# Kernel optimization log

Hardware: AMD Instinct MI355X
Metric: run time of the kernel (lower is better)

## Reference

```python
import jax, jax.numpy as jnp
import numpy as np

E = 1024   # embed_dim
H = 16     # num_heads
D = E // H # head_dim
B = 2
S = 2048
YAT_EPS = 0.1


def setup_inputs() -> dict:
    key = jax.random.key(0)
    ks = jax.random.split(key, 5)
    w_scale = (6.0 / (E + E)) ** 0.5  # xavier_uniform bound
    def xavier(k):
        return jax.random.uniform(k, (E, E), jnp.float32, -w_scale, w_scale)
    return {
        "x": jax.random.normal(ks[0], (B, S, E), jnp.float32),
        "Wq": xavier(ks[1]), "bq": jnp.zeros((E,), jnp.float32),
        "Wk": xavier(ks[2]), "bk": jnp.zeros((E,), jnp.float32),
        "Wv": xavier(ks[3]), "bv": jnp.zeros((E,), jnp.float32),
        "Wo": xavier(ks[4]), "bo": jnp.zeros((E,), jnp.float32),
    }


def reference(x, Wq, bq, Wk, bk, Wv, bv, Wo, bo):
    b, s, _ = x.shape
    # Projections (Linear: x @ W + b, flax kernel layout [in, out])
    Q = x @ Wq + bq
    K = x @ Wk + bk
    V = x @ Wv + bv
    # [B, H, S, D]
    Q = Q.reshape(b, s, H, D).transpose(0, 2, 1, 3)
    K = K.reshape(b, s, H, D).transpose(0, 2, 1, 3)
    V = V.reshape(b, s, H, D).transpose(0, 2, 1, 3)
    # L2 normalize along head_dim
    Qn = Q / (jnp.linalg.norm(Q, axis=-1, keepdims=True) + 1e-8)
    Kn = K / (jnp.linalg.norm(K, axis=-1, keepdims=True) + 1e-8)
    # Yat kernel scores: (1 + <q,k>)^2 / (eps + (1 - <q,k>))
    dot = jnp.einsum("bhqd,bhkd->bhqk", Qn, Kn)
    scores = (1.0 + dot) ** 2 / (YAT_EPS + (1.0 - dot))
    # Sum-normalize (no softmax)
    attn = scores / (jnp.sum(scores, axis=-1, keepdims=True) + 1e-6)
    out = jnp.einsum("bhqk,bhkd->bhqd", attn, V)
    out = out.transpose(0, 2, 1, 3).reshape(b, s, E)
    return out @ Wo + bo
```

## Files before the change

kernel.cpp:

```cpp
#include <hip/hip_runtime.h>
#include <math.h>

#define EDIM 1024
#define NH   16
#define HD   64
#define BATCH 2
#define SEQ  2048
#define NROW (BATCH*SEQ)
#define YAT_EPS 0.1f

typedef _Float16 f16;
typedef _Float16 f16x8 __attribute__((ext_vector_type(8)));
typedef _Float16 f16x4 __attribute__((ext_vector_type(4)));
typedef float    f32x4 __attribute__((ext_vector_type(4)));

#define GLL16(gp, lp) __builtin_amdgcn_global_load_lds( \
    (const __attribute__((address_space(1))) void*)(gp), \
    (__attribute__((address_space(3))) void*)(lp), 16, 0, 0)

__global__ __launch_bounds__(256)
void cast_f16_kernel(const float* __restrict__ src, f16* __restrict__ dst)
{
    const int i = (blockIdx.x * 256 + threadIdx.x) * 4;
    const float4 v = *(const float4*)(src + i);
    f16x4 o = {(f16)v.x, (f16)v.y, (f16)v.z, (f16)v.w};
    *(f16x4*)(dst + i) = o;
}

__global__ __launch_bounds__(256)
void transcast4_kernel(const float* __restrict__ W0, const float* __restrict__ W1,
                       const float* __restrict__ W2, const float* __restrict__ W3,
                       f16* __restrict__ T0, f16* __restrict__ T1,
                       f16* __restrict__ T2, f16* __restrict__ T3)
{
    const int z = blockIdx.z;
    const float* W = (z == 0) ? W0 : (z == 1) ? W1 : (z == 2) ? W2 : W3;
    f16*         Wt = (z == 0) ? T0 : (z == 1) ? T1 : (z == 2) ? T2 : T3;

    __shared__ float T[32][33];
    const int t = threadIdx.x;
    const int r = t >> 3, c4 = (t & 7) * 4;
    const int bi = blockIdx.x * 32, bj = blockIdx.y * 32;
    const float4 v = *(const float4*)(W + (size_t)(bi + r) * 1024 + bj + c4);
    T[r][c4 + 0] = v.x; T[r][c4 + 1] = v.y; T[r][c4 + 2] = v.z; T[r][c4 + 3] = v.w;
    __syncthreads();
    f16x4 o = {(f16)T[c4 + 0][r], (f16)T[c4 + 1][r], (f16)T[c4 + 2][r], (f16)T[c4 + 3][r]};
    *(f16x4*)(Wt + (size_t)(bj + r) * 1024 + bi + c4) = o;
}

__global__ __launch_bounds__(256)
void gemm_f16(const f16* __restrict__ A,
              const f16* __restrict__ B0, const f16* __restrict__ B1, const f16* __restrict__ B2,
              const float* __restrict__ bi0, const float* __restrict__ bi1, const float* __restrict__ bi2,
              void* __restrict__ o0, void* __restrict__ o1, void* __restrict__ o2,
              int e0, int e1, int e2)
{
    __shared__ __align__(16) char lds[24576];

    const int z = blockIdx.z;
    const f16*   Bt   = (z == 0) ? B0  : (z == 1) ? B1  : B2;
    const float* bias = (z == 0) ? bi0 : (z == 1) ? bi1 : bi2;
    void*        Cout = (z == 0) ? o0  : (z == 1) ? o1  : o2;
    const int    epi  = (z == 0) ? e0  : (z == 1) ? e1  : e2;

    const int tid  = threadIdx.x;
    const int lane = tid & 63;
    const int w    = tid >> 6;
    const int cl   = lane & 15;
    const int quad = lane >> 4;
    const int wm = w & 1, wn = w >> 1;
    const int bm = blockIdx.x * 64, bn = blockIdx.y * 128;

    f16* As = (f16*)lds;
    f16* Bs = (f16*)(lds + 8192);

    const int srow = lane >> 2;
    const int scs  = (lane & 3) ^ (srow & 3);
    const f16* gA = A  + (size_t)(bm + w * 16 + srow) * 1024 + scs * 8;
    const f16* gB = Bt + (size_t)(bn + w * 32 + srow) * 1024 + scs * 8;
    f16* lA = As + w * 512;
    f16* lB = Bs + w * 1024;

    f32x4 acc[2][4];
#pragma unroll
    for (int i = 0; i < 2; ++i)
#pragma unroll
        for (int j = 0; j < 4; ++j) acc[i][j] = (f32x4){0.f, 0.f, 0.f, 0.f};

    GLL16(gA, lA);
    GLL16(gB, lB);
    GLL16(gB + 16 * 1024, lB + 512);

    const int fsw = (quad ^ (cl & 3)) * 8;

    for (int it = 0; it < 32; ++it) {
        const int buf = it & 1;
        __syncthreads();
        if (it < 31) {
            const int k0 = (it + 1) * 32;
            const int nb = buf ^ 1;
            GLL16(gA + k0, lA + nb * 2048);
            GLL16(gB + k0, lB + nb * 4096);
            GLL16(gB + 16 * 1024 + k0, lB + nb * 4096 + 512);
        }
        f16x8 af[2], bf[4];
#pragma unroll
        for (int mt = 0; mt < 2; ++mt)
            af[mt] = *(const f16x8*)(&As[buf * 2048 + (wm * 32 + mt * 16 + cl) * 32 + fsw]);
#pragma unroll
        for (int nt = 0; nt < 4; ++nt)
            bf[nt] = *(const f16x8*)(&Bs[buf * 4096 + (wn * 64 + nt * 16 + cl) * 32 + fsw]);
#pragma unroll
        for (int mt = 0; mt < 2; ++mt)
#pragma unroll
            for (int nt = 0; nt < 4; ++nt)
                acc[mt][nt] = __builtin_amdgcn_mfma_f32_16x16x32_f16(af[mt], bf[nt], acc[mt][nt], 0, 0, 0);
    }

    float bcol[4];
#pragma unroll
    for (int nt = 0; nt < 4; ++nt) bcol[nt] = bias[bn + wn * 64 + nt * 16 + cl];
#pragma unroll
    for (int mt = 0; mt < 2; ++mt)
#pragma unroll
        for (int nt = 0; nt < 4; ++nt)
#pragma unroll
            for (int rg = 0; rg < 4; ++rg) acc[mt][nt][rg] += bcol[nt];

    const int b_idx = bm >> 11, sl0 = bm & (SEQ - 1), h0 = bn >> 6;

    if (epi == 0) {
        float* C = (float*)Cout;
#pragma unroll
        for (int mt = 0; mt < 2; ++mt)
#pragma unroll
            for (int rg = 0; rg < 4; ++rg) {
                const int row = bm + wm * 32 + mt * 16 + quad * 4 + rg;
#pragma unroll
                for (int nt = 0; nt < 4; ++nt)
                    C[(size_t)row * EDIM + bn + wn * 64 + nt * 16 + cl] = acc[mt][nt][rg];
            }
    } else if (epi == 1) {
        f16* C = (f16*)Cout;
        __syncthreads();
        f16* S = (f16*)lds;
#pragma unroll
        for (int mt = 0; mt < 2; ++mt)
#pragma unroll
            for (int rg = 0; rg < 4; ++rg) {
                float ss = 0.f;
#pragma unroll
                for (int nt = 0; nt < 4; ++nt) ss += acc[mt][nt][rg] * acc[mt][nt][rg];
                ss += __shfl_xor(ss, 1); ss += __shfl_xor(ss, 2);
                ss += __shfl_xor(ss, 4); ss += __shfl_xor(ss, 8);
                const float inv = 1.0f / (sqrtf(ss) + 1e-8f);
                const int row = wm * 32 + mt * 16 + quad * 4 + rg;
#pragma unroll
                for (int nt = 0; nt < 4; ++nt) {
                    const int col = wn * 64 + nt * 16 + cl;
                    S[row * 128 + (((col >> 3) ^ (row & 15)) * 8) + (col & 7)] =
                        (f16)(acc[mt][nt][rg] * inv);
                }
            }
        __syncthreads();
#pragma unroll
        for (int i = 0; i < 4; ++i) {
            const int c = tid + i * 256;
            const int s = c >> 4, gi = c & 15;
            f16x8 v = *(const f16x8*)(&S[s * 128 + ((gi ^ (s & 15)) * 8)]);
            const int head = h0 + (gi >> 3), d8 = (gi & 7) * 8;
            *(f16x8*)(C + ((size_t)(b_idx * NH + head) * SEQ + sl0 + s) * HD + d8) = v;
        }
    } else {
        f16* C = (f16*)Cout;
        __syncthreads();
        f16* S = (f16*)lds;
#pragma unroll
        for (int mt = 0; mt < 2; ++mt) {
            const int s0 = wm * 32 + mt * 16 + quad * 4;
#pragma unroll
            for (int nt = 0; nt < 4; ++nt) {
                const int col = wn * 64 + nt * 16 + cl;
                f16x4 o = {(f16)acc[mt][nt][0], (f16)acc[mt][nt][1],
                           (f16)acc[mt][nt][2], (f16)acc[mt][nt][3]};
                *(f16x4*)(&S[col * 64 + (((s0 >> 3) ^ (col & 7)) * 8) + (s0 & 7)]) = o;
            }
        }
        __syncthreads();
#pragma unroll
        for (int i = 0; i < 4; ++i) {
            const int c = tid + i * 256;
            const int col = c >> 3, gi = c & 7;
            f16x8 v = *(const f16x8*)(&S[col * 64 + ((gi ^ (col & 7)) * 8)]);
            const int head = h0 + (col >> 6), d = col & 63;
            *(f16x8*)(C + ((size_t)(b_idx * NH + head) * HD + d) * SEQ + sl0 + gi * 8) = v;
        }
    }
}

__global__ __launch_bounds__(256)
void yat_attn(const f16* __restrict__ Qh, const f16* __restrict__ Kh,
              const f16* __restrict__ Vt, f16* __restrict__ AO)
{
    __shared__ __align__(16) char lds[53248];
    f16* KsB = (f16*)(lds + 20480);
    f16* VsB = (f16*)(lds + 36864);

    const int tid  = threadIdx.x;
    const int lane = tid & 63;
    const int w    = tid >> 6;
    const int cl   = lane & 15;
    const int quad = lane >> 4;
    const int wm = w & 1;
    const int wk = w >> 1;
    const int q0 = blockIdx.x * 128;
    const int bh = blockIdx.y;

    const f16* Qg = Qh + (size_t)bh * SEQ * HD;
    const f16* Kg = Kh + (size_t)bh * SEQ * HD;
    const f16* Vg = Vt + (size_t)bh * HD * SEQ;

    const int g8   = lane >> 3;
    const int scs  = (lane & 7) ^ g8;
    const int qrow = w * 8 + g8;
    const int krow = w * 16 + g8;

    {
        const f16* gQ = Qg + (size_t)(q0 + qrow) * HD + scs * 8;
        f16* lQ = (f16*)lds + w * 512;
#pragma unroll
        for (int it = 0; it < 4; ++it)
            GLL16(gQ + it * 32 * HD, lQ + it * 2048);
    }
    __syncthreads();
    f16x8 qf[4][2];
#pragma unroll
    for (int qt = 0; qt < 4; ++qt)
#pragma unroll
        for (int kb = 0; kb < 2; ++kb)
            qf[qt][kb] = *(const f16x8*)((f16*)lds + (wm * 64 + qt * 16 + cl) * 64 +
                                         ((kb * 4 + quad) ^ (cl & 7)) * 8);
    __syncthreads();

    f16* Pw = (f16*)(lds + w * 5120);

    f32x4 O[4][4];
    float rs[4] = {0.f, 0.f, 0.f, 0.f};
#pragma unroll
    for (int i = 0; i < 4; ++i)
#pragma unroll
        for (int j = 0; j < 4; ++j) O[i][j] = (f32x4){0.f, 0.f, 0.f, 0.f};

    const f16* gK = Kg + (size_t)krow * HD + scs * 8;
    const f16* gV = Vg + (size_t)krow * SEQ + scs * 8;
    f16* lK = KsB + w * 1024;
    f16* lV = VsB + w * 1024;

#pragma unroll
    for (int it = 0; it < 2; ++it) {
        GLL16(gK + (size_t)(it * 8) * HD, lK + it * 512);
        GLL16(gV + (size_t)(it * 8) * SEQ, lV + it * 512);
    }

    for (int t0 = 0; t0 < SEQ; t0 += 64) {
        const int buf = (t0 >> 6) & 1;
        __syncthreads();

        if (t0 + 64 < SEQ) {
            const int nb = buf ^ 1;
#pragma unroll
            for (int it = 0; it < 2; ++it) {
                GLL16(gK + (size_t)(t0 + 64 + it * 8) * HD, lK + nb * 4096 + it * 512);
                GLL16(gV + (size_t)(it * 8) * SEQ + t0 + 64, lV + nb * 4096 + it * 512);
            }
        }

        const f16* Ks = KsB + buf * 4096;
        const f16* Vs = VsB + buf * 4096;

        f32x4 s[2][4];
#pragma unroll
        for (int kt = 0; kt < 2; ++kt)
#pragma unroll
            for (int qt = 0; qt < 4; ++qt) s[kt][qt] = (f32x4){0.f, 0.f, 0.f, 0.f};
#pragma unroll
        for (int kb = 0; kb < 2; ++kb) {
            const int sw = ((kb * 4 + quad) ^ (cl & 7)) * 8;
            f16x8 af0 = *(const f16x8*)(&Ks[(wk * 32 +  0 + cl) * 64 + sw]);
            f16x8 af1 = *(const f16x8*)(&Ks[(wk * 32 + 16 + cl) * 64 + sw]);
#pragma unroll
            for (int qt = 0; qt < 4; ++qt) {
                s[0][qt] = __builtin_amdgcn_mfma_f32_16x16x32_f16(af0, qf[qt][kb], s[0][qt], 0, 0, 0);
                s[1][qt] = __builtin_amdgcn_mfma_f32_16x16x32_f16(af1, qf[qt][kb], s[1][qt], 0, 0, 0);
            }
        }

#pragma unroll
        for (int kt = 0; kt < 2; ++kt)
#pragma unroll
            for (int qt = 0; qt < 4; ++qt) {
                f16x4 pk;
                float psum = 0.f;
#pragma unroll
                for (int rg = 0; rg < 4; ++rg) {
                    const float u = (1.0f + YAT_EPS) - s[kt][qt][rg];
                    const float p = fmaf(4.41f, __builtin_amdgcn_rcpf(u), u - 4.2f);
                    psum += p;
                    pk[rg] = (f16)p;
                }
                rs[qt] += psum;
                *(f16x4*)(&Pw[(qt * 16 + cl) * 40 + kt * 16 + quad * 4]) = pk;
            }

        f16x8 pa[4];
#pragma unroll
        for (int qt = 0; qt < 4; ++qt)
            pa[qt] = *(const f16x8*)(&Pw[(qt * 16 + cl) * 40 + quad * 8]);
#pragma unroll
        for (int dn = 0; dn < 4; ++dn) {
            f16x8 vb = *(const f16x8*)(&Vs[(dn * 16 + cl) * 64 +
                                           ((wk * 4 + quad) ^ (cl & 7)) * 8]);
#pragma unroll
            for (int qt = 0; qt < 4; ++qt)
                O[qt][dn] = __builtin_amdgcn_mfma_f32_16x16x32_f16(pa[qt], vb, O[qt][dn], 0, 0, 0);
        }
    }

    __syncthreads();
    float* rs_s = (float*)lds;
    float* Ox   = (float*)(lds + 20480);

#pragma unroll
    for (int qt = 0; qt < 4; ++qt) {
        float t = rs[qt];
        t += __shfl_xor(t, 16);
        t += __shfl_xor(t, 32);
        if (quad == 0) rs_s[wk * 128 + wm * 64 + qt * 16 + cl] = t;
    }
    if (wk == 1) {
#pragma unroll
        for (int qt = 0; qt < 4; ++qt)
#pragma unroll
            for (int dn = 0; dn < 4; ++dn)
#pragma unroll
                for (int rg = 0; rg < 4; ++rg)
                    Ox[(wm * 64 + qt * 16 + quad * 4 + rg) * 64 + dn * 16 + cl] = O[qt][dn][rg];
    }
    __syncthreads();
    if (wk == 0) {
        const int b = bh >> 4, h = bh & 15;
#pragma unroll
        for (int qt = 0; qt < 4; ++qt)
#pragma unroll
            for (int rg = 0; rg < 4; ++rg) {
                const int ql = wm * 64 + qt * 16 + quad * 4 + rg;
                const float tot = rs_s[ql] + rs_s[128 + ql];
                const float inv = 1.0f / (tot + 1e-6f);
                const size_t rowoff = ((size_t)b * SEQ + q0 + ql) * EDIM + h * 64;
#pragma unroll
                for (int dn = 0; dn < 4; ++dn)
                    AO[rowoff + dn * 16 + cl] =
                        (f16)((O[qt][dn][rg] + Ox[ql * 64 + dn * 16 + cl]) * inv);
            }
    }
}

extern "C" void kernel_launch(void* const* d_in, const int* in_sizes, int n_in,
                              void* d_out, int out_size, void* d_ws, size_t ws_size,
                              hipStream_t stream)
{
    const float* x  = (const float*)d_in[0];
    const float* Wq = (const float*)d_in[1];
    const float* bq = (const float*)d_in[2];
    const float* Wk = (const float*)d_in[3];
    const float* bk = (const float*)d_in[4];
    const float* Wv = (const float*)d_in[5];
    const float* bv = (const float*)d_in[6];
    const float* Wo = (const float*)d_in[7];
    const float* bo = (const float*)d_in[8];

    char* p = (char*)d_ws;
    f16* xb  = (f16*)p;                 p += (size_t)NROW * EDIM * 2;
    f16* Wqt = (f16*)p;                 p += (size_t)EDIM * EDIM * 2;
    f16* Wkt = (f16*)p;                 p += (size_t)EDIM * EDIM * 2;
    f16* Wvt = (f16*)p;                 p += (size_t)EDIM * EDIM * 2;
    f16* Wot = (f16*)p;                 p += (size_t)EDIM * EDIM * 2;
    f16* Qhb = (f16*)p;                 p += (size_t)NROW * EDIM * 2;
    f16* Khb = (f16*)p;                 p += (size_t)NROW * EDIM * 2;
    f16* Vtb = (f16*)p;                 p += (size_t)NROW * EDIM * 2;
    f16* AOb = (f16*)p;                 p += (size_t)NROW * EDIM * 2;

    cast_f16_kernel<<<NROW * EDIM / 1024, 256, 0, stream>>>(x, xb);
    transcast4_kernel<<<dim3(32, 32, 4), 256, 0, stream>>>(Wq, Wk, Wv, Wo,
                                                           Wqt, Wkt, Wvt, Wot);

    gemm_f16<<<dim3(NROW / 64, EDIM / 128, 3), 256, 0, stream>>>(
        xb, Wqt, Wkt, Wvt, bq, bk, bv, Qhb, Khb, Vtb, 1, 1, 2);

    yat_attn<<<dim3(SEQ / 128, BATCH * NH), 256, 0, stream>>>(Qhb, Khb, Vtb, AOb);

    gemm_f16<<<dim3(NROW / 64, EDIM / 128, 1), 256, 0, stream>>>(
        AOb, Wot, Wot, Wot, bo, bo, bo, d_out, d_out, d_out, 0, 0, 0);
}
```

Measured before the change: 211.7 us.

## Template GEMM on M-tile and stage loads through registers with deeper prefetch

The GEMM kernel is templated on its M tile size. The QKV projection now uses 128-row tiles, which doubles the MFMA work per B-tile load and halves the grid, while the output projection keeps 64-row tiles. The global_load_lds direct-to-LDS path is replaced by register-staged loads that prefetch two K-steps ahead and write LDS one step ahead, with the barrier moved to the end of each iteration. This adds register pressure, and the larger tile means fewer blocks to fill the GPU.

Result: no change. 209.2 us (-1.2%).

```diff
diff --git a/kernel.cpp b/kernel.cpp
--- a/kernel.cpp
+++ b/kernel.cpp
@@ -48,6 +48,7 @@
     *(f16x4*)(Wt + (size_t)(bj + r) * 1024 + bi + c4) = o;
 }
 
+template<int BM>
 __global__ __launch_bounds__(256)
 void gemm_f16(const f16* __restrict__ A,
               const f16* __restrict__ B0, const f16* __restrict__ B1, const f16* __restrict__ B2,
@@ -55,7 +56,16 @@
               void* __restrict__ o0, void* __restrict__ o1, void* __restrict__ o2,
               int e0, int e1, int e2)
 {
-    __shared__ __align__(16) char lds[24576];
+    constexpr int MT   = BM / 32;
+    constexpr int LA   = BM / 64;
+    constexpr int ABUF = BM * 32;
+    constexpr int BBUF = 128 * 32;
+    constexpr int STG  = 2 * (ABUF + BBUF) * 2;
+    constexpr int EPI  = BM * 128 * 2;
+    constexpr int LDSB = STG > EPI ? STG : EPI;
+    __shared__ __align__(16) char lds[LDSB];
+    f16* As = (f16*)lds;
+    f16* Bs = (f16*)lds + 2 * ABUF;
 
     const int z = blockIdx.z;
     const f16*   Bt   = (z == 0) ? B0  : (z == 1) ? B1  : B2;
@@ -69,59 +79,79 @@
     const int cl   = lane & 15;
     const int quad = lane >> 4;
     const int wm = w & 1, wn = w >> 1;
-    const int bm = blockIdx.x * 64, bn = blockIdx.y * 128;
-
-    f16* As = (f16*)lds;
-    f16* Bs = (f16*)(lds + 8192);
-
-    const int srow = lane >> 2;
-    const int scs  = (lane & 3) ^ (srow & 3);
-    const f16* gA = A  + (size_t)(bm + w * 16 + srow) * 1024 + scs * 8;
-    const f16* gB = Bt + (size_t)(bn + w * 32 + srow) * 1024 + scs * 8;
-    f16* lA = As + w * 512;
-    f16* lB = Bs + w * 1024;
-
-    f32x4 acc[2][4];
-#pragma unroll
-    for (int i = 0; i < 2; ++i)
+    const int bm = blockIdx.x * BM, bn = blockIdx.y * 128;
+    const int wmoff = wm * (MT * 16);
+
+    const int srow = tid >> 2;
+    const int sc   = tid & 3;
+    const int ssw  = (sc ^ (srow & 3)) * 8;
+    const f16* gA = A  + (size_t)(bm + srow) * 1024 + sc * 8;
+    const f16* gB = Bt + (size_t)(bn + srow) * 1024 + sc * 8;
+    int lAo[LA], lBo[2];
+#pragma unroll
+    for (int i = 0; i < LA; ++i) lAo[i] = (srow + i * 64) * 32 + ssw;
+#pragma unroll
+    for (int i = 0; i < 2;  ++i) lBo[i] = (srow + i * 64) * 32 + ssw;
+
+    f32x4 acc[MT][4];
+#pragma unroll
+    for (int i = 0; i < MT; ++i)
 #pragma unroll
         for (int j = 0; j < 4; ++j) acc[i][j] = (f32x4){0.f, 0.f, 0.f, 0.f};
 
-    GLL16(gA, lA);
-    GLL16(gB, lB);
-    GLL16(gB + 16 * 1024, lB + 512);
+    f16x8 ra[LA], rb[2];
+
+#pragma unroll
+    for (int i = 0; i < LA; ++i) ra[i] = *(const f16x8*)(gA + (size_t)i * 64 * 1024);
+#pragma unroll
+    for (int i = 0; i < 2;  ++i) rb[i] = *(const f16x8*)(gB + (size_t)i * 64 * 1024);
+#pragma unroll
+    for (int i = 0; i < LA; ++i) *(f16x8*)(As + lAo[i]) = ra[i];
+#pragma unroll
+    for (int i = 0; i < 2;  ++i) *(f16x8*)(Bs + lBo[i]) = rb[i];
+#pragma unroll
+    for (int i = 0; i < LA; ++i) ra[i] = *(const f16x8*)(gA + (size_t)i * 64 * 1024 + 32);
+#pragma unroll
+    for (int i = 0; i < 2;  ++i) rb[i] = *(const f16x8*)(gB + (size_t)i * 64 * 1024 + 32);
+    __syncthreads();
 
     const int fsw = (quad ^ (cl & 3)) * 8;
 
     for (int it = 0; it < 32; ++it) {
-        const int buf = it & 1;
-        __syncthreads();
+        const int buf = it & 1, nb = buf ^ 1;
         if (it < 31) {
-            const int k0 = (it + 1) * 32;
-            const int nb = buf ^ 1;
-            GLL16(gA + k0, lA + nb * 2048);
-            GLL16(gB + k0, lB + nb * 4096);
-            GLL16(gB + 16 * 1024 + k0, lB + nb * 4096 + 512);
-        }
-        f16x8 af[2], bf[4];
-#pragma unroll
-        for (int mt = 0; mt < 2; ++mt)
-            af[mt] = *(const f16x8*)(&As[buf * 2048 + (wm * 32 + mt * 16 + cl) * 32 + fsw]);
+#pragma unroll
+            for (int i = 0; i < LA; ++i) *(f16x8*)(As + nb * ABUF + lAo[i]) = ra[i];
+#pragma unroll
+            for (int i = 0; i < 2;  ++i) *(f16x8*)(Bs + nb * BBUF + lBo[i]) = rb[i];
+        }
+        if (it < 30) {
+            const int kn = (it + 2) * 32;
+#pragma unroll
+            for (int i = 0; i < LA; ++i) ra[i] = *(const f16x8*)(gA + (size_t)i * 64 * 1024 + kn);
+#pragma unroll
+            for (int i = 0; i < 2;  ++i) rb[i] = *(const f16x8*)(gB + (size_t)i * 64 * 1024 + kn);
+        }
+        f16x8 af[MT], bf[4];
+#pragma unroll
+        for (int mt = 0; mt < MT; ++mt)
+            af[mt] = *(const f16x8*)(&As[buf * ABUF + (wmoff + mt * 16 + cl) * 32 + fsw]);
 #pragma unroll
         for (int nt = 0; nt < 4; ++nt)
-            bf[nt] = *(const f16x8*)(&Bs[buf * 4096 + (wn * 64 + nt * 16 + cl) * 32 + fsw]);
-#pragma unroll
-        for (int mt = 0; mt < 2; ++mt)
+            bf[nt] = *(const f16x8*)(&Bs[buf * BBUF + (wn * 64 + nt * 16 + cl) * 32 + fsw]);
+#pragma unroll
+        for (int mt = 0; mt < MT; ++mt)
 #pragma unroll
             for (int nt = 0; nt < 4; ++nt)
                 acc[mt][nt] = __builtin_amdgcn_mfma_f32_16x16x32_f16(af[mt], bf[nt], acc[mt][nt], 0, 0, 0);
+        __syncthreads();
     }
 
     float bcol[4];
 #pragma unroll
     for (int nt = 0; nt < 4; ++nt) bcol[nt] = bias[bn + wn * 64 + nt * 16 + cl];
 #pragma unroll
-    for (int mt = 0; mt < 2; ++mt)
+    for (int mt = 0; mt < MT; ++mt)
 #pragma unroll
         for (int nt = 0; nt < 4; ++nt)
 #pragma unroll
@@ -132,10 +162,10 @@
     if (epi == 0) {
         float* C = (float*)Cout;
 #pragma unroll
-        for (int mt = 0; mt < 2; ++mt)
+        for (int mt = 0; mt < MT; ++mt)
 #pragma unroll
             for (int rg = 0; rg < 4; ++rg) {
-                const int row = bm + wm * 32 + mt * 16 + quad * 4 + rg;
+                const int row = bm + wmoff + mt * 16 + quad * 4 + rg;
 #pragma unroll
                 for (int nt = 0; nt < 4; ++nt)
                     C[(size_t)row * EDIM + bn + wn * 64 + nt * 16 + cl] = acc[mt][nt][rg];
@@ -145,7 +175,7 @@
         __syncthreads();
         f16* S = (f16*)lds;
 #pragma unroll
-        for (int mt = 0; mt < 2; ++mt)
+        for (int mt = 0; mt < MT; ++mt)
 #pragma unroll
             for (int rg = 0; rg < 4; ++rg) {
                 float ss = 0.f;
@@ -154,7 +184,7 @@
                 ss += __shfl_xor(ss, 1); ss += __shfl_xor(ss, 2);
                 ss += __shfl_xor(ss, 4); ss += __shfl_xor(ss, 8);
                 const float inv = 1.0f / (sqrtf(ss) + 1e-8f);
-                const int row = wm * 32 + mt * 16 + quad * 4 + rg;
+                const int row = wmoff + mt * 16 + quad * 4 + rg;
 #pragma unroll
                 for (int nt = 0; nt < 4; ++nt) {
                     const int col = wn * 64 + nt * 16 + cl;
@@ -164,7 +194,7 @@
             }
         __syncthreads();
 #pragma unroll
-        for (int i = 0; i < 4; ++i) {
+        for (int i = 0; i < BM / 16; ++i) {
             const int c = tid + i * 256;
             const int s = c >> 4, gi = c & 15;
             f16x8 v = *(const f16x8*)(&S[s * 128 + ((gi ^ (s & 15)) * 8)]);
@@ -175,23 +205,25 @@
         f16* C = (f16*)Cout;
         __syncthreads();
         f16* S = (f16*)lds;
-#pragma unroll
-        for (int mt = 0; mt < 2; ++mt) {
-            const int s0 = wm * 32 + mt * 16 + quad * 4;
+        constexpr int GM = BM / 8 - 1;
+#pragma unroll
+        for (int mt = 0; mt < MT; ++mt) {
+            const int s0 = wmoff + mt * 16 + quad * 4;
 #pragma unroll
             for (int nt = 0; nt < 4; ++nt) {
                 const int col = wn * 64 + nt * 16 + cl;
                 f16x4 o = {(f16)acc[mt][nt][0], (f16)acc[mt][nt][1],
                            (f16)acc[mt][nt][2], (f16)acc[mt][nt][3]};
-                *(f16x4*)(&S[col * 64 + (((s0 >> 3) ^ (col & 7)) * 8) + (s0 & 7)]) = o;
-            }
-        }
-        __syncthreads();
-#pragma unroll
-        for (int i = 0; i < 4; ++i) {
+                *(f16x4*)(&S[col * BM + (((s0 >> 3) ^ (col & GM)) * 8) + (s0 & 7)]) = o;
+            }
+        }
+        __syncthreads();
+        constexpr int GSH = (BM == 128) ? 4 : 3;
+#pragma unroll
+        for (int i = 0; i < BM / 16; ++i) {
             const int c = tid + i * 256;
-            const int col = c >> 3, gi = c & 7;
-            f16x8 v = *(const f16x8*)(&S[col * 64 + ((gi ^ (col & 7)) * 8)]);
+            const int col = c >> GSH, gi = c & GM;
+            f16x8 v = *(const f16x8*)(&S[col * BM + ((gi ^ (col & GM)) * 8)]);
             const int head = h0 + (col >> 6), d = col & 63;
             *(f16x8*)(C + ((size_t)(b_idx * NH + head) * HD + d) * SEQ + sl0 + gi * 8) = v;
         }
@@ -394,11 +426,11 @@
     transcast4_kernel<<<dim3(32, 32, 4), 256, 0, stream>>>(Wq, Wk, Wv, Wo,
                                                            Wqt, Wkt, Wvt, Wot);
 
-    gemm_f16<<<dim3(NROW / 64, EDIM / 128, 3), 256, 0, stream>>>(
+    gemm_f16<128><<<dim3(NROW / 128, EDIM / 128, 3), 256, 0, stream>>>(
         xb, Wqt, Wkt, Wvt, bq, bk, bv, Qhb, Khb, Vtb, 1, 1, 2);
 
     yat_attn<<<dim3(SEQ / 128, BATCH * NH), 256, 0, stream>>>(Qhb, Khb, Vtb, AOb);
 
-    gemm_f16<<<dim3(NROW / 64, EDIM / 128, 1), 256, 0, stream>>>(
+    gemm_f16<64><<<dim3(NROW / 64, EDIM / 128, 1), 256, 0, stream>>>(
         AOb, Wot, Wot, Wot, bo, bo, bo, d_out, d_out, d_out, 0, 0, 0);
 }
```
